# Optimization experiments

Measured on AMD Instinct MI355X. Metric: run time of the kernel, lower is better.

The kernel has to match this reference:

```python
import jax, jax.numpy as jnp
import numpy as np

H = 64          # per-direction LSTM hidden
D_IN = 768      # BERT hidden size
D_MODEL = 128   # bidirectional output size


def _lstm_dir(x, W_ih, W_hh, b, reverse):
    # x: [B,S,Din], W_ih: [4H,Din], W_hh: [4H,H], b: [4H]
    B = x.shape[0]
    pre = jnp.einsum('bsd,gd->bsg', x, W_ih) + b  # [B,S,4H]

    def step(carry, p):
        h, c = carry
        g = p + h @ W_hh.T
        i, f, gg, o = jnp.split(g, 4, axis=-1)  # torch gate order i,f,g,o
        c = jax.nn.sigmoid(f) * c + jax.nn.sigmoid(i) * jnp.tanh(gg)
        h = jax.nn.sigmoid(o) * jnp.tanh(c)
        return (h, c), h

    init = (jnp.zeros((B, H), x.dtype), jnp.zeros((B, H), x.dtype))
    _, hs = jax.lax.scan(step, init, jnp.swapaxes(pre, 0, 1), reverse=reverse)
    return jnp.swapaxes(hs, 0, 1)  # [B,S,H]


def _bilstm(x, W_ih, W_hh, b):
    # W_ih: [2,4H,Din] (dir 0 fwd, dir 1 bwd)
    fwd = _lstm_dir(x, W_ih[0], W_hh[0], b[0], False)
    bwd = _lstm_dir(x, W_ih[1], W_hh[1], b[1], True)
    return jnp.concatenate([fwd, bwd], axis=-1)  # [B,S,2H]


def _pool_subwords(subword_emb, word_ids, num_words):
    # scatter-sum subword embeddings into word slots: [B,S,768] -> [B,S,768]
    return jax.vmap(lambda e, i: jax.ops.segment_sum(e, i, num_segments=num_words))(
        subword_emb, word_ids)


def setup_inputs() -> dict:
    key = jax.random.key(0)
    ks = jax.random.split(key, 10)
    B, S = 64, 512
    subword_emb = jax.random.normal(ks[0], (B, S, D_IN), dtype=jnp.float32)
    word_ids_sn = jnp.sort(jax.random.randint(ks[1], (B, S), 0, S, dtype=jnp.int32), axis=1)
    sn_word_len = jax.random.uniform(ks[2], (B, S), dtype=jnp.float32)
    sc = 0.1
    # layer 1: input 768; layers 2-8 (stacked, 7 layers): input 128; combined bias b_ih+b_hh
    W_ih1 = sc * jax.random.normal(ks[3], (2, 4 * H, D_IN), dtype=jnp.float32)
    W_hh1 = sc * jax.random.normal(ks[4], (2, 4 * H, H), dtype=jnp.float32)
    b1 = sc * jax.random.normal(ks[5], (2, 4 * H), dtype=jnp.float32)
    W_ih = sc * jax.random.normal(ks[6], (7, 2, 4 * H, D_MODEL), dtype=jnp.float32)
    W_hh = sc * jax.random.normal(ks[7], (7, 2, 4 * H, H), dtype=jnp.float32)
    b = sc * jax.random.normal(ks[8], (7, 2, 4 * H), dtype=jnp.float32)
    return {"subword_emb": subword_emb, "sn_word_len": sn_word_len,
            "W_ih1": W_ih1, "W_hh1": W_hh1, "b1": b1,
            "W_ih": W_ih, "W_hh": W_hh, "b": b,
            "word_ids_sn": word_ids_sn}


def reference(subword_emb, sn_word_len, W_ih1, W_hh1, b1, W_ih, W_hh, b, word_ids_sn):
    S = subword_emb.shape[1]
    # subword -> word scatter-sum pooling (replaces the per-word-index mask loop)
    merged = _pool_subwords(subword_emb, word_ids_sn, S)        # [B,S,768]
    mask_word = jnp.sum(merged, axis=2).astype(bool)            # [B,S]
    # dropout layers are identity in eval mode
    x = _bilstm(merged, W_ih1, W_hh1, b1)                       # lstm1: 768 -> 128
    x = _bilstm(x, W_ih[0], W_hh[0], b[0])                      # lstm2, no residual
    for l in range(1, 7):                                       # lstm3..lstm8, residual
        x = _bilstm(x, W_ih[l], W_hh[l], b[l]) + x
    out = jnp.concatenate([x, sn_word_len[:, :, None]], axis=2)  # [B,S,129]
    return out, mask_word
```

## Files before the change

kernel.cpp:

```cpp
#include <hip/hip_runtime.h>
#include <math.h>
#include <stdint.h>

#define B 64
#define S 512
#define DIN 768
#define H 64
#define G4 256
#define NG 512
#define DM 128

typedef _Float16 h2_t __attribute__((ext_vector_type(2)));
typedef _Float16 f16x8 __attribute__((ext_vector_type(8)));
typedef float f32x4 __attribute__((ext_vector_type(4)));

#if defined(__has_builtin)
#if __has_builtin(__builtin_amdgcn_fdot2)
#define HAS_FDOT2 1
#endif
#endif

__device__ __forceinline__ h2_t u2h(uint32_t u) {
    h2_t h;
    __builtin_memcpy(&h, &u, 4);
    return h;
}

__device__ __forceinline__ float dot2f(h2_t a, h2_t b, float acc) {
#ifdef HAS_FDOT2
    return __builtin_amdgcn_fdot2(a, b, acc, false);
#else
    acc = fmaf((float)a.x, (float)b.x, acc);
    return fmaf((float)a.y, (float)b.y, acc);
#endif
}

__device__ __forceinline__ float sigm(float x) {
    return 1.0f / (1.0f + __expf(-x));
}
__device__ __forceinline__ float tanh_fast(float x) {
    return 1.0f - 2.0f / (__expf(2.0f * x) + 1.0f);
}

__global__ void pool_kernel(const float* __restrict__ emb,
                            const int* __restrict__ ids,
                            float* __restrict__ merged) {
    int b = blockIdx.x;
    int d = blockIdx.y * 128 + threadIdx.x;
    __shared__ int ids_s[S];
    for (int i = threadIdx.x; i < S; i += blockDim.x) ids_s[i] = ids[b * S + i];
    __syncthreads();
    const float* eb = emb + (size_t)b * S * DIN + d;
    float* mb = merged + (size_t)b * S * DIN + d;
    float acc = 0.f;
    for (int s = 0; s < S; ++s) {
        acc += eb[(size_t)s * DIN];
        int id = ids_s[s];
        bool flush = (s == S - 1) || (ids_s[s + 1] != id);
        if (flush) {
            mb[(size_t)id * DIN] = acc;
            acc = 0.f;
        }
    }
}

__global__ void mask_kernel(const float* __restrict__ merged,
                            float* __restrict__ mask) {
    int row = blockIdx.x * 4 + (threadIdx.x >> 6);
    int lane = threadIdx.x & 63;
    const float* r = merged + (size_t)row * DIN;
    float s = 0.f;
    #pragma unroll
    for (int i = 0; i < DIN / 64; ++i) s += r[lane + i * 64];
    #pragma unroll
    for (int off = 32; off > 0; off >>= 1) s += __shfl_down(s, off);
    if (lane == 0) mask[row] = (s != 0.f) ? 1.0f : 0.0f;
}

#define LDK 40

__global__ __launch_bounds__(256, 2) void gemm_mfma(
    const float* __restrict__ A, int K,
    const float* __restrict__ Wt, const float* __restrict__ bias,
    float* __restrict__ C) {
    __shared__ __align__(16) _Float16 Alds[128][LDK];
    __shared__ __align__(16) _Float16 Blds[64][LDK];
    int tid = threadIdx.x;
    int lane = tid & 63;
    int wave = tid >> 6;
    int wm = wave >> 1, wn = wave & 1;
    int n0 = blockIdx.x * 64;
    int m0 = blockIdx.y * 128;

    int tr = tid >> 2;
    int tc = (tid & 3) << 3;

    f32x4 acc[4][2] = {};

    const float* Ab = A + (size_t)m0 * K;
    for (int k0 = 0; k0 < K; k0 += 32) {
        {
            const float* src = Ab + (size_t)tr * K + k0 + tc;
            float4 v0 = *(const float4*)(src);
            float4 v1 = *(const float4*)(src + 4);
            _Float16* dst = &Alds[tr][tc];
            dst[0] = (_Float16)v0.x; dst[1] = (_Float16)v0.y;
            dst[2] = (_Float16)v0.z; dst[3] = (_Float16)v0.w;
            dst[4] = (_Float16)v1.x; dst[5] = (_Float16)v1.y;
            dst[6] = (_Float16)v1.z; dst[7] = (_Float16)v1.w;
            src += (size_t)64 * K;
            float4 v2 = *(const float4*)(src);
            float4 v3 = *(const float4*)(src + 4);
            dst = &Alds[tr + 64][tc];
            dst[0] = (_Float16)v2.x; dst[1] = (_Float16)v2.y;
            dst[2] = (_Float16)v2.z; dst[3] = (_Float16)v2.w;
            dst[4] = (_Float16)v3.x; dst[5] = (_Float16)v3.y;
            dst[6] = (_Float16)v3.z; dst[7] = (_Float16)v3.w;
        }
        {
            const float* src = Wt + (size_t)(n0 + tr) * K + k0 + tc;
            float4 v0 = *(const float4*)(src);
            float4 v1 = *(const float4*)(src + 4);
            _Float16* dst = &Blds[tr][tc];
            dst[0] = (_Float16)v0.x; dst[1] = (_Float16)v0.y;
            dst[2] = (_Float16)v0.z; dst[3] = (_Float16)v0.w;
            dst[4] = (_Float16)v1.x; dst[5] = (_Float16)v1.y;
            dst[6] = (_Float16)v1.z; dst[7] = (_Float16)v1.w;
        }
        __syncthreads();

        int fr = lane & 15;
        int kg = (lane >> 4) << 3;
        f16x8 af[4], bf[2];
        #pragma unroll
        for (int mf = 0; mf < 4; ++mf)
            af[mf] = *(const f16x8*)&Alds[wm * 64 + mf * 16 + fr][kg];
        #pragma unroll
        for (int nf = 0; nf < 2; ++nf)
            bf[nf] = *(const f16x8*)&Blds[wn * 32 + nf * 16 + fr][kg];
        #pragma unroll
        for (int mf = 0; mf < 4; ++mf)
            #pragma unroll
            for (int nf = 0; nf < 2; ++nf)
                acc[mf][nf] = __builtin_amdgcn_mfma_f32_16x16x32_f16(
                    af[mf], bf[nf], acc[mf][nf], 0, 0, 0);
        __syncthreads();
    }

    int col = lane & 15;
    int r4 = (lane >> 4) << 2;
    #pragma unroll
    for (int nf = 0; nf < 2; ++nf) {
        int n = n0 + wn * 32 + nf * 16 + col;
        float bv = bias[n];
        #pragma unroll
        for (int mf = 0; mf < 4; ++mf) {
            #pragma unroll
            for (int reg = 0; reg < 4; ++reg) {
                int m = m0 + wm * 64 + mf * 16 + r4 + reg;
                C[(size_t)m * NG + n] = acc[mf][nf][reg] + bv;
            }
        }
    }
}

__global__ __launch_bounds__(64, 1) void lstm_rec(
    const float* __restrict__ pre,
    const float* __restrict__ Whh,
    const float* __restrict__ xin,
    float* __restrict__ xout,
    int residual) {
    int b = blockIdx.x >> 1;
    int dir = blockIdx.x & 1;
    int j = threadIdx.x & 63;

    h2_t wg0[32], wg1[32], wg2[32], wg3[32];
    {
        const float* w0 = Whh + (size_t)(dir * G4 + 0 * H + j) * H;
        const float* w1 = Whh + (size_t)(dir * G4 + 1 * H + j) * H;
        const float* w2 = Whh + (size_t)(dir * G4 + 2 * H + j) * H;
        const float* w3 = Whh + (size_t)(dir * G4 + 3 * H + j) * H;
        #pragma unroll
        for (int kk = 0; kk < 32; ++kk) {
            float2 v;
            h2_t p;
            v = *(const float2*)&w0[kk * 2];
            p.x = (_Float16)v.x; p.y = (_Float16)v.y; wg0[kk] = p;
            v = *(const float2*)&w1[kk * 2];
            p.x = (_Float16)v.x; p.y = (_Float16)v.y; wg1[kk] = p;
            v = *(const float2*)&w2[kk * 2];
            p.x = (_Float16)v.x; p.y = (_Float16)v.y; wg2[kk] = p;
            v = *(const float2*)&w3[kk * 2];
            p.x = (_Float16)v.x; p.y = (_Float16)v.y; wg3[kk] = p;
        }
    }

    const float* preb = pre + (size_t)b * S * NG + dir * G4 + j;
    const float* xinb = xin + (size_t)b * S * DM + dir * H + j;
    float* xoutb = xout + (size_t)b * S * DM + dir * H + j;

    float pi[4], pf[4], pg_[4], po[4], rb[4] = {0.f, 0.f, 0.f, 0.f};
    #pragma unroll
    for (int i = 0; i < 4; ++i) {
        int s = dir ? (S - 1 - i) : i;
        const float* p = preb + (size_t)s * NG;
        pi[i] = p[0];
        pf[i] = p[64];
        pg_[i] = p[128];
        po[i] = p[192];
        if (residual) rb[i] = xinb[(size_t)s * DM];
    }

    __shared__ __align__(16) _Float16 shh[64];
    shh[j] = (_Float16)0.f;

    float c = 0.f;
    #pragma unroll 4
    for (int step = 0; step < S; ++step) {
        int s = dir ? (S - 1 - step) : step;
        int q = step & 3;
        float ai = pi[q], af = pf[q], ag = pg_[q], ao = po[q];
        float rv = rb[q];
        int sn = step + 4;
        if (sn < S) {
            int s2 = dir ? (S - 1 - sn) : sn;
            const float* p = preb + (size_t)s2 * NG;
            pi[q] = p[0];
            pf[q] = p[64];
            pg_[q] = p[128];
            po[q] = p[192];
            if (residual) rb[q] = xinb[(size_t)s2 * DM];
        }

        uint4 hq[8];
        const uint4* hp = (const uint4*)shh;
        #pragma unroll
        for (int r = 0; r < 8; ++r) hq[r] = hp[r];

        #pragma unroll
        for (int r = 0; r < 8; ++r) {
            uint32_t uu[4] = {hq[r].x, hq[r].y, hq[r].z, hq[r].w};
            #pragma unroll
            for (int cc = 0; cc < 4; ++cc) {
                int kk = r * 4 + cc;
                h2_t hh = u2h(uu[cc]);
                ai = dot2f(hh, wg0[kk], ai);
                af = dot2f(hh, wg1[kk], af);
                ag = dot2f(hh, wg2[kk], ag);
                ao = dot2f(hh, wg3[kk], ao);
            }
        }
        c = sigm(af) * c + sigm(ai) * tanh_fast(ag);
        float h = sigm(ao) * tanh_fast(c);
        shh[j] = (_Float16)h;
        xoutb[(size_t)s * DM] = h + rv;
    }
}

__global__ void assemble_kernel(const float* __restrict__ x,
                                const float* __restrict__ wl,
                                float* __restrict__ out0) {
    int idx = blockIdx.x * blockDim.x + threadIdx.x;
    if (idx >= B * S * 129) return;
    int c = idx % 129;
    int bs = idx / 129;
    out0[idx] = (c < 128) ? x[(size_t)bs * DM + c] : wl[bs];
}

extern "C" void kernel_launch(void* const* d_in, const int* in_sizes, int n_in,
                              void* d_out, int out_size, void* d_ws, size_t ws_size,
                              hipStream_t stream) {
    const float* emb  = (const float*)d_in[0];
    const float* wl   = (const float*)d_in[1];
    const float* Wih1 = (const float*)d_in[2];
    const float* Whh1 = (const float*)d_in[3];
    const float* b1   = (const float*)d_in[4];
    const float* Wih  = (const float*)d_in[5];
    const float* Whh  = (const float*)d_in[6];
    const float* bb   = (const float*)d_in[7];
    const int*   ids  = (const int*)d_in[8];

    float* out0 = (float*)d_out;
    float* mask_out = out0 + (size_t)B * S * 129;

    float* merged = (float*)d_ws;
    float* pre    = merged + (size_t)B * S * DIN;
    float* xA     = pre + (size_t)B * S * NG;
    float* xB     = xA + (size_t)B * S * DM;

    hipMemsetAsync(merged, 0, (size_t)B * S * DIN * sizeof(float), stream);
    pool_kernel<<<dim3(B, 6), 128, 0, stream>>>(emb, ids, merged);
    mask_kernel<<<(B * S) / 4, 256, 0, stream>>>(merged, mask_out);

    dim3 ggrid(NG / 64, (B * S) / 128);

    gemm_mfma<<<ggrid, 256, 0, stream>>>(merged, DIN, Wih1, b1, pre);
    lstm_rec<<<2 * B, 64, 0, stream>>>(pre, Whh1, nullptr, xA, 0);

    gemm_mfma<<<ggrid, 256, 0, stream>>>(xA, DM, Wih, bb, pre);
    lstm_rec<<<2 * B, 64, 0, stream>>>(pre, Whh, nullptr, xB, 0);

    float* cur = xB;
    float* oth = xA;
    for (int l = 1; l < 7; ++l) {
        gemm_mfma<<<ggrid, 256, 0, stream>>>(cur, DM, Wih + (size_t)l * NG * DM,
                                             bb + (size_t)l * NG, pre);
        lstm_rec<<<2 * B, 64, 0, stream>>>(pre, Whh + (size_t)l * NG * H,
                                           cur, oth, 1);
        float* tmp = cur; cur = oth; oth = tmp;
    }

    assemble_kernel<<<(B * S * 129 + 255) / 256, 256, 0, stream>>>(cur, wl, out0);
}
```

Baseline: 2.685 ms.

## Process two batch rows per LSTM recurrence block to interleave dependency chains

Each recurrence wave now handles two sequences of the same direction, so each weight register is reused for two dot-product chains and the two independent chains can hide each other's latency. The grid is halved from 128 to 64 blocks, which leaves fewer than half the CUs busy. The prefetch depth drops from 4 to 2 steps. Register pressure rises because of the doubled accumulators and h-state loads.

```diff
diff --git a/kernel.cpp b/kernel.cpp
--- a/kernel.cpp
+++ b/kernel.cpp
@@ -170,8 +170,9 @@
     const float* __restrict__ xin,
     float* __restrict__ xout,
     int residual) {
-    int b = blockIdx.x >> 1;
+    int pair = blockIdx.x >> 1;
     int dir = blockIdx.x & 1;
+    int bA = pair * 2, bB = bA + 1;
     int j = threadIdx.x & 63;
 
     h2_t wg0[32], wg1[32], wg2[32], wg3[32];
@@ -195,65 +196,89 @@
         }
     }
 
-    const float* preb = pre + (size_t)b * S * NG + dir * G4 + j;
-    const float* xinb = xin + (size_t)b * S * DM + dir * H + j;
-    float* xoutb = xout + (size_t)b * S * DM + dir * H + j;
-
-    float pi[4], pf[4], pg_[4], po[4], rb[4] = {0.f, 0.f, 0.f, 0.f};
+    const float* prebA = pre + (size_t)bA * S * NG + dir * G4 + j;
+    const float* prebB = pre + (size_t)bB * S * NG + dir * G4 + j;
+    const float* xinbA = xin + (size_t)bA * S * DM + dir * H + j;
+    const float* xinbB = xin + (size_t)bB * S * DM + dir * H + j;
+    float* xoutbA = xout + (size_t)bA * S * DM + dir * H + j;
+    float* xoutbB = xout + (size_t)bB * S * DM + dir * H + j;
+
+    float piA[2], pfA[2], pgA[2], poA[2], rbA[2] = {0.f, 0.f};
+    float piB[2], pfB[2], pgB[2], poB[2], rbB[2] = {0.f, 0.f};
     #pragma unroll
-    for (int i = 0; i < 4; ++i) {
+    for (int i = 0; i < 2; ++i) {
         int s = dir ? (S - 1 - i) : i;
-        const float* p = preb + (size_t)s * NG;
-        pi[i] = p[0];
-        pf[i] = p[64];
-        pg_[i] = p[128];
-        po[i] = p[192];
-        if (residual) rb[i] = xinb[(size_t)s * DM];
-    }
-
-    __shared__ __align__(16) _Float16 shh[64];
+        const float* pA = prebA + (size_t)s * NG;
+        const float* pB = prebB + (size_t)s * NG;
+        piA[i] = pA[0]; pfA[i] = pA[64]; pgA[i] = pA[128]; poA[i] = pA[192];
+        piB[i] = pB[0]; pfB[i] = pB[64]; pgB[i] = pB[128]; poB[i] = pB[192];
+        if (residual) {
+            rbA[i] = xinbA[(size_t)s * DM];
+            rbB[i] = xinbB[(size_t)s * DM];
+        }
+    }
+
+    __shared__ __align__(16) _Float16 shh[128];
+    const uint4* hpA = (const uint4*)&shh[0];
+    const uint4* hpB = (const uint4*)&shh[64];
     shh[j] = (_Float16)0.f;
-
-    float c = 0.f;
-    #pragma unroll 4
+    shh[64 + j] = (_Float16)0.f;
+
+    float cA = 0.f, cB = 0.f;
+    #pragma unroll 2
     for (int step = 0; step < S; ++step) {
         int s = dir ? (S - 1 - step) : step;
-        int q = step & 3;
-        float ai = pi[q], af = pf[q], ag = pg_[q], ao = po[q];
-        float rv = rb[q];
-        int sn = step + 4;
-        if (sn < S) {
-            int s2 = dir ? (S - 1 - sn) : sn;
-            const float* p = preb + (size_t)s2 * NG;
-            pi[q] = p[0];
-            pf[q] = p[64];
-            pg_[q] = p[128];
-            po[q] = p[192];
-            if (residual) rb[q] = xinb[(size_t)s2 * DM];
-        }
-
-        uint4 hq[8];
-        const uint4* hp = (const uint4*)shh;
-        #pragma unroll
-        for (int r = 0; r < 8; ++r) hq[r] = hp[r];
-
+        int q = step & 1;
+
+        uint4 hqA[8], hqB[8];
+        #pragma unroll
+        for (int r = 0; r < 8; ++r) { hqA[r] = hpA[r]; hqB[r] = hpB[r]; }
+
+        float aiA = piA[q], afA = pfA[q], agA = pgA[q], aoA = poA[q];
+        float aiB = piB[q], afB = pfB[q], agB = pgB[q], aoB = poB[q];
         #pragma unroll
         for (int r = 0; r < 8; ++r) {
-            uint32_t uu[4] = {hq[r].x, hq[r].y, hq[r].z, hq[r].w};
+            uint32_t uA[4] = {hqA[r].x, hqA[r].y, hqA[r].z, hqA[r].w};
+            uint32_t uB[4] = {hqB[r].x, hqB[r].y, hqB[r].z, hqB[r].w};
             #pragma unroll
             for (int cc = 0; cc < 4; ++cc) {
                 int kk = r * 4 + cc;
-                h2_t hh = u2h(uu[cc]);
-                ai = dot2f(hh, wg0[kk], ai);
-                af = dot2f(hh, wg1[kk], af);
-                ag = dot2f(hh, wg2[kk], ag);
-                ao = dot2f(hh, wg3[kk], ao);
+                h2_t hA = u2h(uA[cc]);
+                h2_t hB = u2h(uB[cc]);
+                aiA = dot2f(hA, wg0[kk], aiA);
+                aiB = dot2f(hB, wg0[kk], aiB);
+                afA = dot2f(hA, wg1[kk], afA);
+                afB = dot2f(hB, wg1[kk], afB);
+                agA = dot2f(hA, wg2[kk], agA);
+                agB = dot2f(hB, wg2[kk], agB);
+                aoA = dot2f(hA, wg3[kk], aoA);
+                aoB = dot2f(hB, wg3[kk], aoB);
             }
         }
-        c = sigm(af) * c + sigm(ai) * tanh_fast(ag);
-        float h = sigm(ao) * tanh_fast(c);
-        shh[j] = (_Float16)h;
-        xoutb[(size_t)s * DM] = h + rv;
+
+        cA = sigm(afA) * cA + sigm(aiA) * tanh_fast(agA);
+        cB = sigm(afB) * cB + sigm(aiB) * tanh_fast(agB);
+        float hA = sigm(aoA) * tanh_fast(cA);
+        float hB = sigm(aoB) * tanh_fast(cB);
+
+        shh[j] = (_Float16)hA;
+        shh[64 + j] = (_Float16)hB;
+
+        float rvA = rbA[q], rvB = rbB[q];
+        int sn = step + 2;
+        if (sn < S) {
+            int s2 = dir ? (S - 1 - sn) : sn;
+            const float* pA = prebA + (size_t)s2 * NG;
+            const float* pB = prebB + (size_t)s2 * NG;
+            piA[q] = pA[0]; pfA[q] = pA[64]; pgA[q] = pA[128]; poA[q] = pA[192];
+            piB[q] = pB[0]; pfB[q] = pB[64]; pgB[q] = pB[128]; poB[q] = pB[192];
+            if (residual) {
+                rbA[q] = xinbA[(size_t)s2 * DM];
+                rbB[q] = xinbB[(size_t)s2 * DM];
+            }
+        }
+        xoutbA[(size_t)s * DM] = hA + rvA;
+        xoutbB[(size_t)s * DM] = hB + rvB;
     }
 }
 
@@ -295,18 +320,18 @@
     dim3 ggrid(NG / 64, (B * S) / 128);
 
     gemm_mfma<<<ggrid, 256, 0, stream>>>(merged, DIN, Wih1, b1, pre);
-    lstm_rec<<<2 * B, 64, 0, stream>>>(pre, Whh1, nullptr, xA, 0);
+    lstm_rec<<<B, 64, 0, stream>>>(pre, Whh1, nullptr, xA, 0);
 
     gemm_mfma<<<ggrid, 256, 0, stream>>>(xA, DM, Wih, bb, pre);
-    lstm_rec<<<2 * B, 64, 0, stream>>>(pre, Whh, nullptr, xB, 0);
+    lstm_rec<<<B, 64, 0, stream>>>(pre, Whh, nullptr, xB, 0);
 
     float* cur = xB;
     float* oth = xA;
     for (int l = 1; l < 7; ++l) {
         gemm_mfma<<<ggrid, 256, 0, stream>>>(cur, DM, Wih + (size_t)l * NG * DM,
                                              bb + (size_t)l * NG, pre);
-        lstm_rec<<<2 * B, 64, 0, stream>>>(pre, Whh + (size_t)l * NG * H,
-                                           cur, oth, 1);
+        lstm_rec<<<B, 64, 0, stream>>>(pre, Whh + (size_t)l * NG * H,
+                                       cur, oth, 1);
         float* tmp = cur; cur = oth; oth = tmp;
     }
 
```

Measured after the change: 5.052 ms. 88.2% more time.

## Compute LSTM recurrent matvec with MFMA instead of per-lane fp16 dot2

Applied to the files above, without the earlier changes.

The recurrent h·W_hh product in the LSTM step kernel now uses 16x16x32 f16 MFMA instructions. W_hh is held in registers as MFMA B fragments, and h is broadcast into every row of the A operand from shared memory. Each lane then picks its four gate values out of the accumulator tiles. This replaces 128 scalar dot2 instructions per lane per timestep with 32 matrix instructions, aiming to shorten the serial per-step latency. In exchange, 15 of every 16 MFMA rows do redundant work, and a select loop is needed to extract the gate results.

```diff
diff --git a/kernel.cpp b/kernel.cpp
--- a/kernel.cpp
+++ b/kernel.cpp
@@ -13,27 +13,6 @@
 typedef _Float16 h2_t __attribute__((ext_vector_type(2)));
 typedef _Float16 f16x8 __attribute__((ext_vector_type(8)));
 typedef float f32x4 __attribute__((ext_vector_type(4)));
-
-#if defined(__has_builtin)
-#if __has_builtin(__builtin_amdgcn_fdot2)
-#define HAS_FDOT2 1
-#endif
-#endif
-
-__device__ __forceinline__ h2_t u2h(uint32_t u) {
-    h2_t h;
-    __builtin_memcpy(&h, &u, 4);
-    return h;
-}
-
-__device__ __forceinline__ float dot2f(h2_t a, h2_t b, float acc) {
-#ifdef HAS_FDOT2
-    return __builtin_amdgcn_fdot2(a, b, acc, false);
-#else
-    acc = fmaf((float)a.x, (float)b.x, acc);
-    return fmaf((float)a.y, (float)b.y, acc);
-#endif
-}
 
 __device__ __forceinline__ float sigm(float x) {
     return 1.0f / (1.0f + __expf(-x));
@@ -173,25 +152,26 @@
     int b = blockIdx.x >> 1;
     int dir = blockIdx.x & 1;
     int j = threadIdx.x & 63;
-
-    h2_t wg0[32], wg1[32], wg2[32], wg3[32];
+    int c15 = j & 15;
+    int kg = (j >> 4) << 3;
+
+    f16x8 bf[16][2];
     {
-        const float* w0 = Whh + (size_t)(dir * G4 + 0 * H + j) * H;
-        const float* w1 = Whh + (size_t)(dir * G4 + 1 * H + j) * H;
-        const float* w2 = Whh + (size_t)(dir * G4 + 2 * H + j) * H;
-        const float* w3 = Whh + (size_t)(dir * G4 + 3 * H + j) * H;
-        #pragma unroll
-        for (int kk = 0; kk < 32; ++kk) {
-            float2 v;
-            h2_t p;
-            v = *(const float2*)&w0[kk * 2];
-            p.x = (_Float16)v.x; p.y = (_Float16)v.y; wg0[kk] = p;
-            v = *(const float2*)&w1[kk * 2];
-            p.x = (_Float16)v.x; p.y = (_Float16)v.y; wg1[kk] = p;
-            v = *(const float2*)&w2[kk * 2];
-            p.x = (_Float16)v.x; p.y = (_Float16)v.y; wg2[kk] = p;
-            v = *(const float2*)&w3[kk * 2];
-            p.x = (_Float16)v.x; p.y = (_Float16)v.y; wg3[kk] = p;
+        const float* wbase = Whh + (size_t)dir * G4 * H;
+        #pragma unroll
+        for (int t = 0; t < 16; ++t) {
+            const float* row = wbase + (size_t)(16 * t + c15) * H;
+            #pragma unroll
+            for (int hh = 0; hh < 2; ++hh) {
+                float4 v0 = *(const float4*)(row + hh * 32 + kg);
+                float4 v1 = *(const float4*)(row + hh * 32 + kg + 4);
+                f16x8 f;
+                f[0] = (_Float16)v0.x; f[1] = (_Float16)v0.y;
+                f[2] = (_Float16)v0.z; f[3] = (_Float16)v0.w;
+                f[4] = (_Float16)v1.x; f[5] = (_Float16)v1.y;
+                f[6] = (_Float16)v1.z; f[7] = (_Float16)v1.w;
+                bf[t][hh] = f;
+            }
         }
     }
 
@@ -214,12 +194,42 @@
     __shared__ __align__(16) _Float16 shh[64];
     shh[j] = (_Float16)0.f;
 
+    int tq = j >> 4;
     float c = 0.f;
     #pragma unroll 4
     for (int step = 0; step < S; ++step) {
         int s = dir ? (S - 1 - step) : step;
         int q = step & 3;
-        float ai = pi[q], af = pf[q], ag = pg_[q], ao = po[q];
+
+        f16x8 af0 = *(const f16x8*)&shh[kg];
+        f16x8 af1 = *(const f16x8*)&shh[32 + kg];
+
+        f32x4 acc[16] = {};
+        #pragma unroll
+        for (int t = 0; t < 16; ++t) {
+            acc[t] = __builtin_amdgcn_mfma_f32_16x16x32_f16(af0, bf[t][0],
+                                                            acc[t], 0, 0, 0);
+            acc[t] = __builtin_amdgcn_mfma_f32_16x16x32_f16(af1, bf[t][1],
+                                                            acc[t], 0, 0, 0);
+        }
+
+        float gi = 0.f, gf = 0.f, gg = 0.f, go = 0.f;
+        #pragma unroll
+        for (int tt = 0; tt < 4; ++tt) {
+            if (tq == tt) {
+                gi = acc[tt][0];
+                gf = acc[4 + tt][0];
+                gg = acc[8 + tt][0];
+                go = acc[12 + tt][0];
+            }
+        }
+        gi += pi[q]; gf += pf[q]; gg += pg_[q]; go += po[q];
+
+        c = sigm(gf) * c + sigm(gi) * tanh_fast(gg);
+        float h = sigm(go) * tanh_fast(c);
+
+        shh[j] = (_Float16)h;
+
         float rv = rb[q];
         int sn = step + 4;
         if (sn < S) {
@@ -231,28 +241,6 @@
             po[q] = p[192];
             if (residual) rb[q] = xinb[(size_t)s2 * DM];
         }
-
-        uint4 hq[8];
-        const uint4* hp = (const uint4*)shh;
-        #pragma unroll
-        for (int r = 0; r < 8; ++r) hq[r] = hp[r];
-
-        #pragma unroll
-        for (int r = 0; r < 8; ++r) {
-            uint32_t uu[4] = {hq[r].x, hq[r].y, hq[r].z, hq[r].w};
-            #pragma unroll
-            for (int cc = 0; cc < 4; ++cc) {
-                int kk = r * 4 + cc;
-                h2_t hh = u2h(uu[cc]);
-                ai = dot2f(hh, wg0[kk], ai);
-                af = dot2f(hh, wg1[kk], af);
-                ag = dot2f(hh, wg2[kk], ag);
-                ao = dot2f(hh, wg3[kk], ao);
-            }
-        }
-        c = sigm(af) * c + sigm(ai) * tanh_fast(ag);
-        float h = sigm(ao) * tanh_fast(c);
-        shh[j] = (_Float16)h;
         xoutb[(size_t)s * DM] = h + rv;
     }
 }
```

Measured after the change: 3.660 ms. 1.36x slower.
